# Optimization experiments

Measured on AMD Instinct MI355X. Metric: run time of the kernel, lower is better.

The kernel has to match this reference:

```python
import jax, jax.numpy as jnp
import numpy as np

EPS = 1e-5
N_HEAD = 16

def _ln(x, g, b):
    m = jnp.mean(x, -1, keepdims=True)
    v = jnp.mean((x - m) ** 2, -1, keepdims=True)
    return (x - m) * jax.lax.rsqrt(v + EPS) * g + b

def _mlp(x, fc_w, fc_b, proj_w, proj_b):
    h = x @ fc_w.T + fc_b
    h = h * jax.nn.sigmoid(1.702 * h)  # QuickGELU
    return h @ proj_w.T + proj_b

def setup_inputs() -> dict:
    key = jax.random.key(0)
    ks = jax.random.split(key, 16)
    S, B, D, BOX = 577, 8, 1024, 16
    sc = 0.02
    return {
        'x': jax.random.normal(ks[0], (S, B, D), jnp.float32),
        'detection_attn_mask': jax.random.normal(ks[1], (B * BOX * N_HEAD, 1, S), jnp.float32),
        'box_coords': jax.random.uniform(ks[2], (B, BOX, 4), jnp.float32),
        'layers': 24,
        'need_patch': 0,
        'in_proj_w': sc * jax.random.normal(ks[3], (3 * D, D), jnp.float32),
        'in_proj_b': jnp.zeros((3 * D,), jnp.float32),
        'out_w': sc * jax.random.normal(ks[4], (D, D), jnp.float32),
        'out_b': jnp.zeros((D,), jnp.float32),
        'ln1_g': jnp.ones((D,), jnp.float32),
        'ln1_b': jnp.zeros((D,), jnp.float32),
        'ln2_g': jnp.ones((D,), jnp.float32),
        'ln2_b': jnp.zeros((D,), jnp.float32),
        'fc_w': sc * jax.random.normal(ks[5], (4 * D, D), jnp.float32),
        'fc_b': jnp.zeros((4 * D,), jnp.float32),
        'proj_w': sc * jax.random.normal(ks[6], (D, 4 * D), jnp.float32),
        'proj_b': jnp.zeros((D,), jnp.float32),
    }

def reference(x, detection_attn_mask, box_coords, layers, need_patch,
              in_proj_w, in_proj_b, out_w, out_b,
              ln1_g, ln1_b, ln2_g, ln2_b, fc_w, fc_b, proj_w, proj_b):
    # step == layers-1, detection_attn_mask is not None, need_patch is False.
    S, B, D = x.shape
    H = N_HEAD
    hd = D // H
    BOX = box_coords.shape[1]  # uniform boxes per image

    h = _ln(x, ln1_g, ln1_b)                       # [S,B,D]
    qkv = h @ in_proj_w.T + in_proj_b              # [S,B,3D]
    q, k, v = jnp.split(qkv, 3, axis=-1)

    # query is sliced to the CLS token only (q[:, :1, :] after head split)
    q0 = q[0].reshape(B, H, hd) / jnp.sqrt(jnp.asarray(hd, x.dtype))  # [B,H,hd]
    kh = k.reshape(S, B, H, hd).transpose(1, 2, 0, 3)                 # [B,H,S,hd]
    vh = v.reshape(S, B, H, hd).transpose(1, 2, 0, 3)                 # [B,H,S,hd]

    attn = jnp.einsum('bhe,bhse->bhs', q0, kh)     # [B,H,S]

    # mask rows are ordered (batch, box, head); Nt == 1 is squeezed
    mask = detection_attn_mask.reshape(B, BOX, H, S)
    p_exp = jax.nn.softmax(attn[:, None] + mask, axis=-1)             # [B,BOX,H,S]
    out_exp = jnp.einsum('bxhs,bhse->bxhe', p_exp, vh).reshape(B * BOX, D)
    out_exp = out_exp @ out_w.T + out_b            # [B*BOX, D]

    p = jax.nn.softmax(attn, axis=-1)
    out = jnp.einsum('bhs,bhse->bhe', p, vh).reshape(B, D) @ out_w.T + out_b

    cls = x[0] + out                               # residual with CLS token
    cls = cls + _mlp(_ln(cls, ln2_g, ln2_b), fc_w, fc_b, proj_w, proj_b)

    x0_exp = jnp.repeat(x[0], BOX, axis=0)         # [B*BOX, D], batch-major
    mask_cls = x0_exp + out_exp
    mask_cls = mask_cls + _mlp(_ln(mask_cls, ln2_g, ln2_b), fc_w, fc_b, proj_w, proj_b)

    return mask_cls[None], cls[None]               # [1,B*BOX,D], [1,B,D]
```

## Files before the change

kernel.cpp:

```cpp
#include <hip/hip_runtime.h>
#include <stdint.h>

typedef unsigned short u16;
typedef unsigned int u32;
typedef __bf16 bf16x8 __attribute__((ext_vector_type(8)));
typedef float f32x4 __attribute__((ext_vector_type(4)));

__device__ __forceinline__ float bf2f(u16 u) {
  u32 v = ((u32)u) << 16;
  return __builtin_bit_cast(float, v);
}
__device__ __forceinline__ u16 f2bf(float f) {
  u32 u = __builtin_bit_cast(u32, f);
  u32 r = u + 0x7fffu + ((u >> 16) & 1u);
  return (u16)(r >> 16);
}

__device__ __forceinline__ float block_sum4(float v, float* red, int t) {
#pragma unroll
  for (int o = 32; o; o >>= 1) v += __shfl_xor(v, o, 64);
  if ((t & 63) == 0) red[t >> 6] = v;
  __syncthreads();
  float r = red[0] + red[1] + red[2] + red[3];
  __syncthreads();
  return r;
}

#define GLD16(gp, lp)                                                   \
  __builtin_amdgcn_global_load_lds(                                     \
      (const __attribute__((address_space(1))) void*)(gp),              \
      (__attribute__((address_space(3))) void*)(lp), 16, 0, 0)

struct CvtSegs {
  const float* src[5];
  u16* dst[5];
  int nblk[6];
};
__global__ __launch_bounds__(256) void cvt_all(CvtSegs segs) {
  int blk = blockIdx.x;
  int s = 0;
  while (s < 4 && blk >= segs.nblk[s + 1]) ++s;
  int i = (blk - segs.nblk[s]) * 1024 + threadIdx.x * 4;
  float4 f = *(const float4*)(segs.src[s] + i);
  u32 lo = (u32)f2bf(f.x) | ((u32)f2bf(f.y) << 16);
  u32 hi = (u32)f2bf(f.z) | ((u32)f2bf(f.w) << 16);
  uint2 val = {lo, hi};
  *(uint2*)(segs.dst[s] + i) = val;
}

__global__ __launch_bounds__(256) void ln_rows_f32(
    const float* __restrict__ X, const float* __restrict__ G,
    const float* __restrict__ Bt, u16* __restrict__ O) {
  __shared__ float red[4];
  int row = blockIdx.x, t = threadIdx.x;
  float4 xv = *(const float4*)(X + (size_t)row * 1024 + t * 4);
  float v[4] = {xv.x, xv.y, xv.z, xv.w};
  float s = v[0] + v[1] + v[2] + v[3];
  s = block_sum4(s, red, t);
  float mean = s * (1.f / 1024.f);
  float q = 0.f;
#pragma unroll
  for (int i = 0; i < 4; ++i) { float d = v[i] - mean; q += d * d; }
  q = block_sum4(q, red, t);
  float rstd = rsqrtf(q * (1.f / 1024.f) + 1e-5f);
  float4 g = *(const float4*)(G + t * 4);
  float4 b = *(const float4*)(Bt + t * 4);
  float gg[4] = {g.x, g.y, g.z, g.w}, bb[4] = {b.x, b.y, b.z, b.w};
  u16 o[4];
#pragma unroll
  for (int i = 0; i < 4; ++i) o[i] = f2bf((v[i] - mean) * rstd * gg[i] + bb[i]);
  u32* op = (u32*)(O + (size_t)row * 1024 + t * 4);
  op[0] = (u32)o[0] | ((u32)o[1] << 16);
  op[1] = (u32)o[2] | ((u32)o[3] << 16);
}

__global__ __launch_bounds__(256) void resid_ln_red(
    const float* __restrict__ X, const float* __restrict__ OP,
    const float* __restrict__ OB, const float* __restrict__ G,
    const float* __restrict__ Bt, float* __restrict__ CLS, u16* __restrict__ H2) {
  __shared__ float red[4];
  const int PS = 136 * 1024;
  int row = blockIdx.x, t = threadIdx.x;
  int bi = (row < 128) ? (row >> 4) : (row - 128);
  float4 xv = *(const float4*)(X + (size_t)bi * 1024 + t * 4);
  float4 ob = *(const float4*)(OB + t * 4);
  float v[4] = {xv.x + ob.x, xv.y + ob.y, xv.z + ob.z, xv.w + ob.w};
#pragma unroll
  for (int z = 0; z < 8; ++z) {
    float4 pv = *(const float4*)(OP + (size_t)z * PS + (size_t)row * 1024 + t * 4);
    v[0] += pv.x; v[1] += pv.y; v[2] += pv.z; v[3] += pv.w;
  }
  float* cp = CLS + (size_t)row * 1024 + t * 4;
#pragma unroll
  for (int i = 0; i < 4; ++i) cp[i] = v[i];
  float s = v[0] + v[1] + v[2] + v[3];
  s = block_sum4(s, red, t);
  float mean = s * (1.f / 1024.f);
  float q = 0.f;
#pragma unroll
  for (int i = 0; i < 4; ++i) { float d = v[i] - mean; q += d * d; }
  q = block_sum4(q, red, t);
  float rstd = rsqrtf(q * (1.f / 1024.f) + 1e-5f);
  float4 g = *(const float4*)(G + t * 4);
  float4 b = *(const float4*)(Bt + t * 4);
  float gg[4] = {g.x, g.y, g.z, g.w}, bb[4] = {b.x, b.y, b.z, b.w};
  u16 o[4];
#pragma unroll
  for (int i = 0; i < 4; ++i) o[i] = f2bf((v[i] - mean) * rstd * gg[i] + bb[i]);
  u32* op = (u32*)(H2 + (size_t)row * 1024 + t * 4);
  op[0] = (u32)o[0] | ((u32)o[1] << 16);
  op[1] = (u32)o[2] | ((u32)o[3] << 16);
}

__global__ __launch_bounds__(256) void gemm_bt_128(
    const u16* __restrict__ A, int lda, const u16* __restrict__ W, int ldw,
    const float* __restrict__ bias, u16* __restrict__ C, int ldc,
    int M, int N, int K) {
  __shared__ u16 As[128 * 64];
  __shared__ u16 Bs[128 * 64];
  int t = threadIdx.x, lane = t & 63, wv = t >> 6;
  int bm = blockIdx.x * 128, bn = blockIdx.y * 128;
  int quad = lane >> 4, rlow = lane & 15;
  int lrow = lane >> 3, lcol = (lane & 7) * 8;
  int wrow = (wv & 1) * 64, wcol = (wv >> 1) * 64;
  f32x4 acc[4][4] = {};

  for (int k0 = 0; k0 < K; k0 += 64) {
    __syncthreads();
#pragma unroll
    for (int j = 0; j < 4; ++j) {
      int rb = j * 4 + wv;
      int row = rb * 8 + lrow;
      int gm = bm + row; if (gm >= M) gm = M - 1;
      GLD16(A + (size_t)gm * lda + k0 + lcol, &As[rb * 8 * 64]);
      int gn = bn + row; if (gn >= N) gn = N - 1;
      GLD16(W + (size_t)gn * ldw + k0 + lcol, &Bs[rb * 8 * 64]);
    }
    __syncthreads();
#pragma unroll
    for (int kk = 0; kk < 64; kk += 32) {
      bf16x8 a[4], b[4];
#pragma unroll
      for (int i = 0; i < 4; ++i)
        a[i] = *(const bf16x8*)(&As[(wrow + i * 16 + rlow) * 64 + kk + quad * 8]);
#pragma unroll
      for (int j = 0; j < 4; ++j)
        b[j] = *(const bf16x8*)(&Bs[(wcol + j * 16 + rlow) * 64 + kk + quad * 8]);
#pragma unroll
      for (int i = 0; i < 4; ++i)
#pragma unroll
        for (int j = 0; j < 4; ++j)
          acc[i][j] = __builtin_amdgcn_mfma_f32_16x16x32_bf16(a[i], b[j], acc[i][j], 0, 0, 0);
    }
  }
#pragma unroll
  for (int j = 0; j < 4; ++j) {
    int gn = bn + wcol + j * 16 + rlow;
    float bv = (gn < N) ? bias[gn] : 0.f;
#pragma unroll
    for (int i = 0; i < 4; ++i)
#pragma unroll
      for (int r = 0; r < 4; ++r) {
        int gm = bm + wrow + i * 16 + quad * 4 + r;
        if (gm < M && gn < N) C[(size_t)gm * ldc + gn] = f2bf(acc[i][j][r] + bv);
      }
  }
}

#define LDT 72
__global__ __launch_bounds__(256) void gemm_bt_splitk_p(
    const u16* __restrict__ A, int lda, const u16* __restrict__ W, int ldw,
    float* __restrict__ P, int pstride, int ldc, int M, int N, int KC) {
  __shared__ u16 As[64 * LDT];
  __shared__ u16 Bs[64 * LDT];
  int t = threadIdx.x;
  int bm = blockIdx.x * 64, bn = blockIdx.y * 64;
  int kbase = blockIdx.z * KC;
  float* PZ = P + (size_t)blockIdx.z * pstride;
  int lane = t & 63, wv = t >> 6;
  f32x4 acc[4] = {};
  int srow = t >> 3;
  int scol = (t & 7) * 8;

  for (int k0 = kbase; k0 < kbase + KC; k0 += 64) {
    __syncthreads();
#pragma unroll
    for (int rr = 0; rr < 2; ++rr) {
      int r = srow + rr * 32;
      int gm = bm + r;
      uint4 da = {0, 0, 0, 0};
      if (gm < M) da = *(const uint4*)(A + (size_t)gm * lda + k0 + scol);
      *(uint4*)(&As[r * LDT + scol]) = da;
      int gn = bn + r;
      uint4 dw = {0, 0, 0, 0};
      if (gn < N) dw = *(const uint4*)(W + (size_t)gn * ldw + k0 + scol);
      *(uint4*)(&Bs[r * LDT + scol]) = dw;
    }
    __syncthreads();
    int quad = lane >> 4, rlow = lane & 15;
#pragma unroll
    for (int kk = 0; kk < 64; kk += 32) {
      bf16x8 a = *(const bf16x8*)(&As[(wv * 16 + rlow) * LDT + kk + quad * 8]);
#pragma unroll
      for (int j = 0; j < 4; ++j) {
        bf16x8 b = *(const bf16x8*)(&Bs[(j * 16 + rlow) * LDT + kk + quad * 8]);
        acc[j] = __builtin_amdgcn_mfma_f32_16x16x32_bf16(a, b, acc[j], 0, 0, 0);
      }
    }
  }
  int quad = lane >> 4, cidx = lane & 15;
#pragma unroll
  for (int j = 0; j < 4; ++j) {
    int gn = bn + j * 16 + cidx;
#pragma unroll
    for (int r = 0; r < 4; ++r) {
      int gm = bm + wv * 16 + quad * 4 + r;
      if (gm < M && gn < N) PZ[(size_t)gm * ldc + gn] = acc[j][r];
    }
  }
}

__global__ __launch_bounds__(256) void gelu_red(
    const float* __restrict__ FP, const float* __restrict__ FB,
    u16* __restrict__ O, int total) {
  const int PS = 136 * 4096;
  int i = (blockIdx.x * 256 + threadIdx.x) * 4;
  if (i < total) {
#pragma unroll
    for (int k = 0; k < 4; ++k) {
      int idx = i + k;
      float v = FB[idx & 4095];
#pragma unroll
      for (int z = 0; z < 4; ++z) v += FP[(size_t)z * PS + idx];
      O[idx] = f2bf(v / (1.f + __expf(-1.702f * v)));
    }
  }
}

__global__ __launch_bounds__(256) void final_red(
    const float* __restrict__ PP, const float* __restrict__ PB,
    const float* __restrict__ CLS, float* __restrict__ O, int total) {
  const int PS = 136 * 1024;
  int i = (blockIdx.x * 256 + threadIdx.x) * 4;
  if (i < total) {
#pragma unroll
    for (int k = 0; k < 4; ++k) {
      int idx = i + k;
      float v = PB[idx & 1023] + CLS[idx];
#pragma unroll
      for (int z = 0; z < 16; ++z) v += PP[(size_t)z * PS + idx];
      O[idx] = v;
    }
  }
}

__global__ __launch_bounds__(256) void qw_build(
    const float* __restrict__ QP, const float* __restrict__ QB,
    const float* __restrict__ WK, const float* __restrict__ BK,
    u16* __restrict__ QW, float* __restrict__ C0) {
  const int PS = 8 * 1024;
  int bh = blockIdx.x, b = bh >> 4, h = bh & 15;
  __shared__ float qs[64];
  int t = threadIdx.x;
  if (t < 64) {
    int n = h * 64 + t;
    float q = QB[n];
#pragma unroll
    for (int z = 0; z < 8; ++z) q += QP[(size_t)z * PS + b * 1024 + n];
    qs[t] = q * 0.125f;
  }
  __syncthreads();
  float acc[4] = {0.f, 0.f, 0.f, 0.f};
  int d0 = t * 4;
#pragma unroll 4
  for (int n = 0; n < 64; ++n) {
    float4 w = *(const float4*)(WK + (size_t)(h * 64 + n) * 1024 + d0);
    float q = qs[n];
    acc[0] += q * w.x;
    acc[1] += q * w.y;
    acc[2] += q * w.z;
    acc[3] += q * w.w;
  }
  u16 o[4];
#pragma unroll
  for (int i = 0; i < 4; ++i) o[i] = f2bf(acc[i]);
  u32* op = (u32*)(QW + (size_t)bh * 1024 + d0);
  op[0] = (u32)o[0] | ((u32)o[1] << 16);
  op[1] = (u32)o[2] | ((u32)o[3] << 16);
  if (t == 0) {
    float c = 0.f;
    for (int n = 0; n < 64; ++n) c += qs[n] * BK[h * 64 + n];
    C0[bh] = c;
  }
}

#define HLD 516
__global__ __launch_bounds__(256) void attn_dot(
    const u16* __restrict__ H, const u16* __restrict__ QW,
    const float* __restrict__ C0, float* __restrict__ ATT) {
  __shared__ u32 Hs[16 * HLD];
  int b = blockIdx.y, s0 = blockIdx.x * 16, t = threadIdx.x;
  for (int idx = t; idx < 16 * 512; idx += 256) {
    int row = idx >> 9, col = idx & 511;
    int s = s0 + row;
    u32 v = 0;
    if (s < 577) v = *(const u32*)(H + ((size_t)(s * 8 + b) << 10) + col * 2);
    Hs[row * HLD + col] = v;
  }
  __syncthreads();
  int si = t & 15, hh = t >> 4;
  int s = s0 + si;
  if (s < 577) {
    const u32* hr = &Hs[si * HLD];
    const u32* qr = (const u32*)(QW + (size_t)(b * 16 + hh) * 1024);
    float acc = 0.f;
    for (int d = 0; d < 512; d += 4) {
      uint4 hv = *(const uint4*)(&hr[d]);
      uint4 qv = *(const uint4*)(&qr[d]);
      acc += bf2f(hv.x & 0xffff) * bf2f(qv.x & 0xffff) + bf2f(hv.x >> 16) * bf2f(qv.x >> 16);
      acc += bf2f(hv.y & 0xffff) * bf2f(qv.y & 0xffff) + bf2f(hv.y >> 16) * bf2f(qv.y >> 16);
      acc += bf2f(hv.z & 0xffff) * bf2f(qv.z & 0xffff) + bf2f(hv.z >> 16) * bf2f(qv.z >> 16);
      acc += bf2f(hv.w & 0xffff) * bf2f(qv.w & 0xffff) + bf2f(hv.w >> 16) * bf2f(qv.w >> 16);
    }
    ATT[(size_t)(b * 16 + hh) * 577 + s] = acc + C0[b * 16 + hh];
  }
}

__global__ __launch_bounds__(256) void softmax_pv(
    const float* __restrict__ ATT, const float* __restrict__ MASK,
    const u16* __restrict__ V, u16* __restrict__ AO) {
  const int S = 577;
  int blk = blockIdx.x;
  int b = blk / 272, rem = blk % 272;
  int x = rem >> 4, h = rem & 15;
  __shared__ float p[S];
  __shared__ float redm[4];
  __shared__ float reds[4];
  __shared__ float partial[256];
  int t = threadIdx.x, lane = t & 63, wv = t >> 6;
  const float* arow = ATT + (size_t)(b * 16 + h) * S;
  float lmax = -3e38f;
  for (int s = t; s < S; s += 256) {
    float v = arow[s];
    if (x < 16) v += MASK[(size_t)((b * 16 + x) * 16 + h) * S + s];
    p[s] = v;
    lmax = fmaxf(lmax, v);
  }
#pragma unroll
  for (int o = 32; o; o >>= 1) lmax = fmaxf(lmax, __shfl_xor(lmax, o, 64));
  if (lane == 0) redm[wv] = lmax;
  __syncthreads();
  float m = fmaxf(fmaxf(redm[0], redm[1]), fmaxf(redm[2], redm[3]));
  float lsum = 0.f;
  for (int s = t; s < S; s += 256) {
    float e = __expf(p[s] - m);
    p[s] = e;
    lsum += e;
  }
#pragma unroll
  for (int o = 32; o; o >>= 1) lsum += __shfl_xor(lsum, o, 64);
  if (lane == 0) reds[wv] = lsum;
  __syncthreads();
  float inv = 1.f / (reds[0] + reds[1] + reds[2] + reds[3]);
  float acc = 0.f;
  const u16* vb = V + h * 64 + lane;
  int s = wv;
  for (; s + 28 < S; s += 32) {
    float w0 = p[s], w1 = p[s + 4], w2 = p[s + 8], w3 = p[s + 12];
    float w4 = p[s + 16], w5 = p[s + 20], w6 = p[s + 24], w7 = p[s + 28];
    float v0 = bf2f(vb[(size_t)((s)*8 + b) << 10]);
    float v1 = bf2f(vb[(size_t)((s + 4) * 8 + b) << 10]);
    float v2 = bf2f(vb[(size_t)((s + 8) * 8 + b) << 10]);
    float v3 = bf2f(vb[(size_t)((s + 12) * 8 + b) << 10]);
    float v4 = bf2f(vb[(size_t)((s + 16) * 8 + b) << 10]);
    float v5 = bf2f(vb[(size_t)((s + 20) * 8 + b) << 10]);
    float v6 = bf2f(vb[(size_t)((s + 24) * 8 + b) << 10]);
    float v7 = bf2f(vb[(size_t)((s + 28) * 8 + b) << 10]);
    acc += w0 * v0 + w1 * v1 + w2 * v2 + w3 * v3;
    acc += w4 * v4 + w5 * v5 + w6 * v6 + w7 * v7;
  }
  for (; s < S; s += 4) acc += p[s] * bf2f(vb[(size_t)(s * 8 + b) << 10]);
  partial[t] = acc;
  __syncthreads();
  if (t < 64) {
    float r = (partial[t] + partial[t + 64] + partial[t + 128] + partial[t + 192]) * inv;
    int row = (x < 16) ? (b * 16 + x) : (128 + b);
    AO[(size_t)row * 1024 + h * 64 + t] = f2bf(r);
  }
}

extern "C" void kernel_launch(void* const* d_in, const int* in_sizes, int n_in,
                              void* d_out, int out_size, void* d_ws, size_t ws_size,
                              hipStream_t stream) {
  const float* x      = (const float*)d_in[0];
  const float* mask   = (const float*)d_in[1];
  const float* in_w   = (const float*)d_in[5];
  const float* in_b   = (const float*)d_in[6];
  const float* out_w  = (const float*)d_in[7];
  const float* out_b  = (const float*)d_in[8];
  const float* ln1_g  = (const float*)d_in[9];
  const float* ln1_b  = (const float*)d_in[10];
  const float* ln2_g  = (const float*)d_in[11];
  const float* ln2_b  = (const float*)d_in[12];
  const float* fc_w   = (const float*)d_in[13];
  const float* fc_b   = (const float*)d_in[14];
  const float* proj_w = (const float*)d_in[15];
  const float* proj_b = (const float*)d_in[16];
  float* out = (float*)d_out;

  const int SB = 577 * 8;
  char* base = (char*)d_ws;
  size_t off = 0;
  auto alloc = [&](size_t bytes) {
    char* p = base + off;
    off += (bytes + 255) & ~(size_t)255;
    return p;
  };
  u16* wq_b    = (u16*)alloc((size_t)1024 * 1024 * 2);
  u16* wv_b    = (u16*)alloc((size_t)1024 * 1024 * 2);
  u16* wout_b  = (u16*)alloc((size_t)1024 * 1024 * 2);
  u16* wfc_b   = (u16*)alloc((size_t)4096 * 1024 * 2);
  u16* wproj_b = (u16*)alloc((size_t)4096 * 1024 * 2);
  u16* h        = (u16*)alloc((size_t)SB * 1024 * 2);
  u16* v        = (u16*)alloc((size_t)SB * 1024 * 2);
  float* Qp     = (float*)alloc((size_t)8 * 8 * 1024 * 4);
  u16* qw       = (u16*)alloc(128 * 1024 * 2);
  float* c0     = (float*)alloc(128 * 4);
  float* attn   = (float*)alloc(128 * 577 * 4);
  u16* attn_out = (u16*)alloc(136 * 1024 * 2);
  float* Op     = (float*)alloc((size_t)8 * 136 * 1024 * 4);
  float* clspre = (float*)alloc(136 * 1024 * 4);
  u16* h2       = (u16*)alloc(136 * 1024 * 2);
  float* Fp     = (float*)alloc((size_t)4 * 136 * 4096 * 4);
  u16* hg       = (u16*)alloc((size_t)136 * 4096 * 2);
  float* Pp     = (float*)alloc((size_t)16 * 136 * 1024 * 4);

  CvtSegs segs;
  segs.src[0] = in_w;                      segs.dst[0] = wq_b;
  segs.src[1] = in_w + (size_t)2048*1024;  segs.dst[1] = wv_b;
  segs.src[2] = out_w;                     segs.dst[2] = wout_b;
  segs.src[3] = fc_w;                      segs.dst[3] = wfc_b;
  segs.src[4] = proj_w;                    segs.dst[4] = wproj_b;
  segs.nblk[0] = 0;    segs.nblk[1] = 1024; segs.nblk[2] = 2048;
  segs.nblk[3] = 3072; segs.nblk[4] = 7168; segs.nblk[5] = 11264;
  cvt_all<<<11264, 256, 0, stream>>>(segs);

  ln_rows_f32<<<SB, 256, 0, stream>>>(x, ln1_g, ln1_b, h);
  gemm_bt_128<<<dim3(37, 8), 256, 0, stream>>>(
      h, 1024, wv_b, 1024, in_b + 2048, v, 1024, SB, 1024, 1024);
  gemm_bt_splitk_p<<<dim3(1, 16, 8), 256, 0, stream>>>(
      h, 1024, wq_b, 1024, Qp, 8 * 1024, 1024, 8, 1024, 128);
  qw_build<<<128, 256, 0, stream>>>(Qp, in_b, in_w + (size_t)1024 * 1024,
                                    in_b + 1024, qw, c0);
  attn_dot<<<dim3(37, 8), 256, 0, stream>>>(h, qw, c0, attn);
  softmax_pv<<<8 * 17 * 16, 256, 0, stream>>>(attn, mask, v, attn_out);
  gemm_bt_splitk_p<<<dim3(3, 16, 8), 256, 0, stream>>>(
      attn_out, 1024, wout_b, 1024, Op, 136 * 1024, 1024, 136, 1024, 128);
  resid_ln_red<<<136, 256, 0, stream>>>(x, Op, out_b, ln2_g, ln2_b, clspre, h2);
  gemm_bt_splitk_p<<<dim3(3, 64, 4), 256, 0, stream>>>(
      h2, 1024, wfc_b, 1024, Fp, 136 * 4096, 4096, 136, 4096, 256);
  gelu_red<<<544, 256, 0, stream>>>(Fp, fc_b, hg, 136 * 4096);
  gemm_bt_splitk_p<<<dim3(3, 16, 16), 256, 0, stream>>>(
      hg, 4096, wproj_b, 4096, Pp, 136 * 1024, 1024, 136, 1024, 256);
  final_red<<<136, 256, 0, stream>>>(Pp, proj_b, clspre, out, 136 * 1024);

  (void)in_sizes; (void)n_in; (void)out_size; (void)ws_size;
}
```

Before: 267.6 us.

## Convert weights to bf16 inside GEMM loads and fuse Q projection into qw build

Drops the up-front conversion of the Q, out, fc and proj weights to bf16. The split-K GEMM now reads fp32 weights directly and rounds them to bf16 while staging into shared memory, which removes a separate pass that wrote and re-read a bf16 copy. The CLS-token Q projection is computed inside a fused kernel with fp32 dot products, replacing a split-K GEMM plus reduction. Each weight GEMM now reads twice as many bytes, since the rows are fp32, and does conversion ALU work in its load path.

```diff
diff --git a/kernel.cpp b/kernel.cpp
--- a/kernel.cpp
+++ b/kernel.cpp
@@ -6,6 +6,9 @@
 typedef __bf16 bf16x8 __attribute__((ext_vector_type(8)));
 typedef float f32x4 __attribute__((ext_vector_type(4)));
 
+#define LDT 72
+#define HLD 516
+
 __device__ __forceinline__ float bf2f(u16 u) {
   u32 v = ((u32)u) << 16;
   return __builtin_bit_cast(float, v);
@@ -31,21 +34,14 @@
       (const __attribute__((address_space(1))) void*)(gp),              \
       (__attribute__((address_space(3))) void*)(lp), 16, 0, 0)
 
-struct CvtSegs {
-  const float* src[5];
-  u16* dst[5];
-  int nblk[6];
-};
-__global__ __launch_bounds__(256) void cvt_all(CvtSegs segs) {
-  int blk = blockIdx.x;
-  int s = 0;
-  while (s < 4 && blk >= segs.nblk[s + 1]) ++s;
-  int i = (blk - segs.nblk[s]) * 1024 + threadIdx.x * 4;
-  float4 f = *(const float4*)(segs.src[s] + i);
+__global__ __launch_bounds__(256) void cvt_f32_bf16(
+    const float* __restrict__ S, u16* __restrict__ D) {
+  int i = blockIdx.x * 1024 + threadIdx.x * 4;
+  float4 f = *(const float4*)(S + i);
   u32 lo = (u32)f2bf(f.x) | ((u32)f2bf(f.y) << 16);
   u32 hi = (u32)f2bf(f.z) | ((u32)f2bf(f.w) << 16);
   uint2 val = {lo, hi};
-  *(uint2*)(segs.dst[s] + i) = val;
+  *(uint2*)(D + i) = val;
 }
 
 __global__ __launch_bounds__(256) void ln_rows_f32(
@@ -70,44 +66,6 @@
 #pragma unroll
   for (int i = 0; i < 4; ++i) o[i] = f2bf((v[i] - mean) * rstd * gg[i] + bb[i]);
   u32* op = (u32*)(O + (size_t)row * 1024 + t * 4);
-  op[0] = (u32)o[0] | ((u32)o[1] << 16);
-  op[1] = (u32)o[2] | ((u32)o[3] << 16);
-}
-
-__global__ __launch_bounds__(256) void resid_ln_red(
-    const float* __restrict__ X, const float* __restrict__ OP,
-    const float* __restrict__ OB, const float* __restrict__ G,
-    const float* __restrict__ Bt, float* __restrict__ CLS, u16* __restrict__ H2) {
-  __shared__ float red[4];
-  const int PS = 136 * 1024;
-  int row = blockIdx.x, t = threadIdx.x;
-  int bi = (row < 128) ? (row >> 4) : (row - 128);
-  float4 xv = *(const float4*)(X + (size_t)bi * 1024 + t * 4);
-  float4 ob = *(const float4*)(OB + t * 4);
-  float v[4] = {xv.x + ob.x, xv.y + ob.y, xv.z + ob.z, xv.w + ob.w};
-#pragma unroll
-  for (int z = 0; z < 8; ++z) {
-    float4 pv = *(const float4*)(OP + (size_t)z * PS + (size_t)row * 1024 + t * 4);
-    v[0] += pv.x; v[1] += pv.y; v[2] += pv.z; v[3] += pv.w;
-  }
-  float* cp = CLS + (size_t)row * 1024 + t * 4;
-#pragma unroll
-  for (int i = 0; i < 4; ++i) cp[i] = v[i];
-  float s = v[0] + v[1] + v[2] + v[3];
-  s = block_sum4(s, red, t);
-  float mean = s * (1.f / 1024.f);
-  float q = 0.f;
-#pragma unroll
-  for (int i = 0; i < 4; ++i) { float d = v[i] - mean; q += d * d; }
-  q = block_sum4(q, red, t);
-  float rstd = rsqrtf(q * (1.f / 1024.f) + 1e-5f);
-  float4 g = *(const float4*)(G + t * 4);
-  float4 b = *(const float4*)(Bt + t * 4);
-  float gg[4] = {g.x, g.y, g.z, g.w}, bb[4] = {b.x, b.y, b.z, b.w};
-  u16 o[4];
-#pragma unroll
-  for (int i = 0; i < 4; ++i) o[i] = f2bf((v[i] - mean) * rstd * gg[i] + bb[i]);
-  u32* op = (u32*)(H2 + (size_t)row * 1024 + t * 4);
   op[0] = (u32)o[0] | ((u32)o[1] << 16);
   op[1] = (u32)o[2] | ((u32)o[3] << 16);
 }
@@ -167,9 +125,8 @@
   }
 }
 
-#define LDT 72
 __global__ __launch_bounds__(256) void gemm_bt_splitk_p(
-    const u16* __restrict__ A, int lda, const u16* __restrict__ W, int ldw,
+    const u16* __restrict__ A, int lda, const float* __restrict__ Wf, int ldw,
     float* __restrict__ P, int pstride, int ldc, int M, int N, int KC) {
   __shared__ u16 As[64 * LDT];
   __shared__ u16 Bs[64 * LDT];
@@ -179,8 +136,7 @@
   float* PZ = P + (size_t)blockIdx.z * pstride;
   int lane = t & 63, wv = t >> 6;
   f32x4 acc[4] = {};
-  int srow = t >> 3;
-  int scol = (t & 7) * 8;
+  int srow = t >> 3, scol = (t & 7) * 8;
 
   for (int k0 = kbase; k0 < kbase + KC; k0 += 64) {
     __syncthreads();
@@ -193,7 +149,15 @@
       *(uint4*)(&As[r * LDT + scol]) = da;
       int gn = bn + r;
       uint4 dw = {0, 0, 0, 0};
-      if (gn < N) dw = *(const uint4*)(W + (size_t)gn * ldw + k0 + scol);
+      if (gn < N) {
+        const float* wr = Wf + (size_t)gn * ldw + k0 + scol;
+        float4 w0 = *(const float4*)(wr);
+        float4 w1 = *(const float4*)(wr + 4);
+        dw.x = (u32)f2bf(w0.x) | ((u32)f2bf(w0.y) << 16);
+        dw.y = (u32)f2bf(w0.z) | ((u32)f2bf(w0.w) << 16);
+        dw.z = (u32)f2bf(w1.x) | ((u32)f2bf(w1.y) << 16);
+        dw.w = (u32)f2bf(w1.z) | ((u32)f2bf(w1.w) << 16);
+      }
       *(uint4*)(&Bs[r * LDT + scol]) = dw;
     }
     __syncthreads();
@@ -218,6 +182,44 @@
       if (gm < M && gn < N) PZ[(size_t)gm * ldc + gn] = acc[j][r];
     }
   }
+}
+
+__global__ __launch_bounds__(256) void resid_ln_red(
+    const float* __restrict__ X, const float* __restrict__ OP,
+    const float* __restrict__ OB, const float* __restrict__ G,
+    const float* __restrict__ Bt, float* __restrict__ CLS, u16* __restrict__ H2) {
+  __shared__ float red[4];
+  const int PS = 136 * 1024;
+  int row = blockIdx.x, t = threadIdx.x;
+  int bi = (row < 128) ? (row >> 4) : (row - 128);
+  float4 xv = *(const float4*)(X + (size_t)bi * 1024 + t * 4);
+  float4 ob = *(const float4*)(OB + t * 4);
+  float v[4] = {xv.x + ob.x, xv.y + ob.y, xv.z + ob.z, xv.w + ob.w};
+#pragma unroll
+  for (int z = 0; z < 8; ++z) {
+    float4 pv = *(const float4*)(OP + (size_t)z * PS + (size_t)row * 1024 + t * 4);
+    v[0] += pv.x; v[1] += pv.y; v[2] += pv.z; v[3] += pv.w;
+  }
+  float* cp = CLS + (size_t)row * 1024 + t * 4;
+#pragma unroll
+  for (int i = 0; i < 4; ++i) cp[i] = v[i];
+  float s = v[0] + v[1] + v[2] + v[3];
+  s = block_sum4(s, red, t);
+  float mean = s * (1.f / 1024.f);
+  float q = 0.f;
+#pragma unroll
+  for (int i = 0; i < 4; ++i) { float d = v[i] - mean; q += d * d; }
+  q = block_sum4(q, red, t);
+  float rstd = rsqrtf(q * (1.f / 1024.f) + 1e-5f);
+  float4 g = *(const float4*)(G + t * 4);
+  float4 b = *(const float4*)(Bt + t * 4);
+  float gg[4] = {g.x, g.y, g.z, g.w}, bb[4] = {b.x, b.y, b.z, b.w};
+  u16 o[4];
+#pragma unroll
+  for (int i = 0; i < 4; ++i) o[i] = f2bf((v[i] - mean) * rstd * gg[i] + bb[i]);
+  u32* op = (u32*)(H2 + (size_t)row * 1024 + t * 4);
+  op[0] = (u32)o[0] | ((u32)o[1] << 16);
+  op[1] = (u32)o[2] | ((u32)o[3] << 16);
 }
 
 __global__ __launch_bounds__(256) void gelu_red(
@@ -254,47 +256,62 @@
   }
 }
 
-__global__ __launch_bounds__(256) void qw_build(
-    const float* __restrict__ QP, const float* __restrict__ QB,
-    const float* __restrict__ WK, const float* __restrict__ BK,
-    u16* __restrict__ QW, float* __restrict__ C0) {
-  const int PS = 8 * 1024;
+__global__ __launch_bounds__(256) void q_fused(
+    const u16* __restrict__ H, const float* __restrict__ WQ,
+    const float* __restrict__ QB, const float* __restrict__ WK,
+    const float* __restrict__ BK, u16* __restrict__ QW, float* __restrict__ C0) {
+  __shared__ float hsf[1024];
+  __shared__ float ps[256];
+  __shared__ float qs[64];
   int bh = blockIdx.x, b = bh >> 4, h = bh & 15;
-  __shared__ float qs[64];
   int t = threadIdx.x;
+  {
+    uint2 two = *(const uint2*)(H + (size_t)b * 1024 + t * 4);
+    hsf[t * 4 + 0] = bf2f(two.x & 0xffff);
+    hsf[t * 4 + 1] = bf2f(two.x >> 16);
+    hsf[t * 4 + 2] = bf2f(two.y & 0xffff);
+    hsf[t * 4 + 3] = bf2f(two.y >> 16);
+  }
+  __syncthreads();
+  {
+    int n = t >> 2, part = t & 3;
+    const float* wr = WQ + (size_t)(h * 64 + n) * 1024 + part * 256;
+    const float* hp = hsf + part * 256;
+    float acc = 0.f;
+#pragma unroll 4
+    for (int d = 0; d < 256; d += 4) {
+      float4 w = *(const float4*)(wr + d);
+      acc += w.x * hp[d] + w.y * hp[d + 1] + w.z * hp[d + 2] + w.w * hp[d + 3];
+    }
+    ps[t] = acc;
+  }
+  __syncthreads();
   if (t < 64) {
-    int n = h * 64 + t;
-    float q = QB[n];
-#pragma unroll
-    for (int z = 0; z < 8; ++z) q += QP[(size_t)z * PS + b * 1024 + n];
+    float q = ps[t * 4] + ps[t * 4 + 1] + ps[t * 4 + 2] + ps[t * 4 + 3] + QB[h * 64 + t];
     qs[t] = q * 0.125f;
   }
   __syncthreads();
-  float acc[4] = {0.f, 0.f, 0.f, 0.f};
+  float a4[4] = {0.f, 0.f, 0.f, 0.f};
   int d0 = t * 4;
 #pragma unroll 4
-  for (int n = 0; n < 64; ++n) {
-    float4 w = *(const float4*)(WK + (size_t)(h * 64 + n) * 1024 + d0);
-    float q = qs[n];
-    acc[0] += q * w.x;
-    acc[1] += q * w.y;
-    acc[2] += q * w.z;
-    acc[3] += q * w.w;
+  for (int n2 = 0; n2 < 64; ++n2) {
+    float4 w = *(const float4*)(WK + (size_t)(h * 64 + n2) * 1024 + d0);
+    float q = qs[n2];
+    a4[0] += q * w.x; a4[1] += q * w.y; a4[2] += q * w.z; a4[3] += q * w.w;
   }
   u16 o[4];
 #pragma unroll
-  for (int i = 0; i < 4; ++i) o[i] = f2bf(acc[i]);
+  for (int i = 0; i < 4; ++i) o[i] = f2bf(a4[i]);
   u32* op = (u32*)(QW + (size_t)bh * 1024 + d0);
   op[0] = (u32)o[0] | ((u32)o[1] << 16);
   op[1] = (u32)o[2] | ((u32)o[3] << 16);
   if (t == 0) {
     float c = 0.f;
-    for (int n = 0; n < 64; ++n) c += qs[n] * BK[h * 64 + n];
+    for (int n2 = 0; n2 < 64; ++n2) c += qs[n2] * BK[h * 64 + n2];
     C0[bh] = c;
   }
 }
 
-#define HLD 516
 __global__ __launch_bounds__(256) void attn_dot(
     const u16* __restrict__ H, const u16* __restrict__ QW,
     const float* __restrict__ C0, float* __restrict__ ATT) {
@@ -416,14 +433,9 @@
     off += (bytes + 255) & ~(size_t)255;
     return p;
   };
-  u16* wq_b    = (u16*)alloc((size_t)1024 * 1024 * 2);
-  u16* wv_b    = (u16*)alloc((size_t)1024 * 1024 * 2);
-  u16* wout_b  = (u16*)alloc((size_t)1024 * 1024 * 2);
-  u16* wfc_b   = (u16*)alloc((size_t)4096 * 1024 * 2);
-  u16* wproj_b = (u16*)alloc((size_t)4096 * 1024 * 2);
+  u16* wv_b     = (u16*)alloc((size_t)1024 * 1024 * 2);
   u16* h        = (u16*)alloc((size_t)SB * 1024 * 2);
   u16* v        = (u16*)alloc((size_t)SB * 1024 * 2);
-  float* Qp     = (float*)alloc((size_t)8 * 8 * 1024 * 4);
   u16* qw       = (u16*)alloc(128 * 1024 * 2);
   float* c0     = (float*)alloc(128 * 4);
   float* attn   = (float*)alloc(128 * 577 * 4);
@@ -435,33 +447,22 @@
   u16* hg       = (u16*)alloc((size_t)136 * 4096 * 2);
   float* Pp     = (float*)alloc((size_t)16 * 136 * 1024 * 4);
 
-  CvtSegs segs;
-  segs.src[0] = in_w;                      segs.dst[0] = wq_b;
-  segs.src[1] = in_w + (size_t)2048*1024;  segs.dst[1] = wv_b;
-  segs.src[2] = out_w;                     segs.dst[2] = wout_b;
-  segs.src[3] = fc_w;                      segs.dst[3] = wfc_b;
-  segs.src[4] = proj_w;                    segs.dst[4] = wproj_b;
-  segs.nblk[0] = 0;    segs.nblk[1] = 1024; segs.nblk[2] = 2048;
-  segs.nblk[3] = 3072; segs.nblk[4] = 7168; segs.nblk[5] = 11264;
-  cvt_all<<<11264, 256, 0, stream>>>(segs);
-
+  cvt_f32_bf16<<<1024, 256, 0, stream>>>(in_w + (size_t)2048 * 1024, wv_b);
   ln_rows_f32<<<SB, 256, 0, stream>>>(x, ln1_g, ln1_b, h);
   gemm_bt_128<<<dim3(37, 8), 256, 0, stream>>>(
       h, 1024, wv_b, 1024, in_b + 2048, v, 1024, SB, 1024, 1024);
-  gemm_bt_splitk_p<<<dim3(1, 16, 8), 256, 0, stream>>>(
-      h, 1024, wq_b, 1024, Qp, 8 * 1024, 1024, 8, 1024, 128);
-  qw_build<<<128, 256, 0, stream>>>(Qp, in_b, in_w + (size_t)1024 * 1024,
-                                    in_b + 1024, qw, c0);
+  q_fused<<<128, 256, 0, stream>>>(h, in_w, in_b, in_w + (size_t)1024 * 1024,
+                                   in_b + 1024, qw, c0);
   attn_dot<<<dim3(37, 8), 256, 0, stream>>>(h, qw, c0, attn);
   softmax_pv<<<8 * 17 * 16, 256, 0, stream>>>(attn, mask, v, attn_out);
   gemm_bt_splitk_p<<<dim3(3, 16, 8), 256, 0, stream>>>(
-      attn_out, 1024, wout_b, 1024, Op, 136 * 1024, 1024, 136, 1024, 128);
+      attn_out, 1024, out_w, 1024, Op, 136 * 1024, 1024, 136, 1024, 128);
   resid_ln_red<<<136, 256, 0, stream>>>(x, Op, out_b, ln2_g, ln2_b, clspre, h2);
   gemm_bt_splitk_p<<<dim3(3, 64, 4), 256, 0, stream>>>(
-      h2, 1024, wfc_b, 1024, Fp, 136 * 4096, 4096, 136, 4096, 256);
+      h2, 1024, fc_w, 1024, Fp, 136 * 4096, 4096, 136, 4096, 256);
   gelu_red<<<544, 256, 0, stream>>>(Fp, fc_b, hg, 136 * 4096);
   gemm_bt_splitk_p<<<dim3(3, 16, 16), 256, 0, stream>>>(
-      hg, 4096, wproj_b, 4096, Pp, 136 * 1024, 1024, 136, 1024, 256);
+      hg, 4096, proj_w, 4096, Pp, 136 * 1024, 1024, 136, 1024, 256);
   final_red<<<136, 256, 0, stream>>>(Pp, proj_b, clspre, out, 136 * 1024);
 
   (void)in_sizes; (void)n_in; (void)out_size; (void)ws_size;
```

After: 268.0 us. No clear change (+0.1%).
